# Performance work log

Hardware: AMD Instinct MI355X
Metric: run time of the kernel (lower is better)

## Reference

```python
import jax, jax.numpy as jnp
import numpy as np

BN_EPS = 1e-5

def _bn_train(h, gamma, beta):
    # BatchNorm1d in training mode: batch statistics over the node dim
    mean = jnp.mean(h, axis=0)
    var = jnp.mean((h - mean) ** 2, axis=0)  # biased variance, as torch BN uses for normalization
    return gamma * (h - mean) * jax.lax.rsqrt(var + BN_EPS) + beta


def setup_inputs() -> dict:
    key = jax.random.key(0)
    ks = jax.random.split(key, 8)
    N, E = 100000, 1250000
    d_in, d_out = 64, 128
    x = jax.random.normal(ks[0], (N, d_in), dtype=jnp.float32)
    edge_index = jax.random.randint(ks[1], (2, E), 0, N, dtype=jnp.int64)
    s1 = 1.0 / np.sqrt(d_in)
    s2 = 1.0 / np.sqrt(d_out)
    W1 = jax.random.uniform(ks[2], (d_in, d_out), dtype=jnp.float32, minval=-s1, maxval=s1)
    b1 = jax.random.uniform(ks[3], (d_out,), dtype=jnp.float32, minval=-s1, maxval=s1)
    g1 = jnp.ones((d_out,), dtype=jnp.float32)
    be1 = jnp.zeros((d_out,), dtype=jnp.float32)
    W2 = jax.random.uniform(ks[4], (d_out, d_out), dtype=jnp.float32, minval=-s2, maxval=s2)
    b2 = jax.random.uniform(ks[5], (d_out,), dtype=jnp.float32, minval=-s2, maxval=s2)
    g2 = jnp.ones((d_out,), dtype=jnp.float32)
    be2 = jnp.zeros((d_out,), dtype=jnp.float32)
    return {"x": x, "edge_index": edge_index, "W1": W1, "b1": b1, "g1": g1, "be1": be1,
            "W2": W2, "b2": b2, "g2": g2, "be2": be2}


def reference(x, edge_index, W1, b1, g1, be1, W2, b2, g2, be2):
    src = edge_index[0]
    dst = edge_index[1]
    N = x.shape[0]
    # GIN aggregation: sum of neighbor features scattered to destination nodes
    agg = jax.ops.segment_sum(x[src], dst, num_segments=N)
    h = x + agg  # (1 + eps) * x + agg with eps = 0 (GINConv default)
    # MLP: Linear -> ReLU -> BN -> Linear -> ReLU -> BN
    h = jnp.maximum(h @ W1 + b1, 0.0)
    h = _bn_train(h, g1, be1)
    h = jnp.maximum(h @ W2 + b2, 0.0)
    h = _bn_train(h, g2, be2)
    return h
```

## Files before the change

### kernel.cpp

```cpp
#include <hip/hip_runtime.h>


#define NBMAX 512
#define CAP   8192
#define CPB   4096

__global__ __launch_bounds__(512) void k_zero(int* __restrict__ gcnt,
                                              float* __restrict__ stats)
{
    int t = threadIdx.x;
    gcnt[t] = 0;
    stats[t] = 0.f;
}

__global__ __launch_bounds__(256) void k_part(const int* __restrict__ ei, int E,
                                              int* __restrict__ gcnt,
                                              unsigned int* __restrict__ pk)
{
    __shared__ int cnt[NBMAX];
    __shared__ int gbase[NBMAX];
    const int tid = threadIdx.x;
    const int e0 = blockIdx.x * CPB;
    const int e1 = min(E, e0 + CPB);

    for (int i = tid; i < NBMAX; i += 256) cnt[i] = 0;
    __syncthreads();

    for (int e = e0 + tid; e < e1; e += 256)
        atomicAdd(&cnt[ei[E + e] >> 8], 1);
    __syncthreads();

    for (int i = tid; i < NBMAX; i += 256)
        gbase[i] = cnt[i] ? atomicAdd(&gcnt[i], cnt[i]) : 0;
    __syncthreads();
    for (int i = tid; i < NBMAX; i += 256) cnt[i] = 0;
    __syncthreads();

    for (int e = e0 + tid; e < e1; e += 256) {
        int dst = ei[E + e];
        int src = ei[e];
        int b = dst >> 8;
        int lr = atomicAdd(&cnt[b], 1);
        pk[(long)b * CAP + gbase[b] + lr] =
            ((unsigned)(dst & 255) << 17) | (unsigned)src;
    }
}

__global__ __launch_bounds__(256) void k_csr(const unsigned int* __restrict__ pk,
                                             const int* __restrict__ gcnt,
                                             int* __restrict__ nbr,
                                             int* __restrict__ beg,
                                             int* __restrict__ endq, int N)
{
    __shared__ int lcnt[256];
    __shared__ int lscan[256];
    const int tid = threadIdx.x;
    const int b = blockIdx.x;
    const int cnt = gcnt[b];
    const unsigned int* eb = pk + (long)b * CAP;

    lcnt[tid] = 0;
    __syncthreads();
    for (int j = tid; j < cnt; j += 256)
        atomicAdd(&lcnt[eb[j] >> 17], 1);
    __syncthreads();

    int v = lcnt[tid];
    lscan[tid] = v;
    __syncthreads();
    for (int off = 1; off < 256; off <<= 1) {
        int t = (tid >= off) ? lscan[tid - off] : 0;
        __syncthreads();
        lscan[tid] += t;
        __syncthreads();
    }
    int excl = lscan[tid] - v;

    int node = (b << 8) + tid;
    if (node < N) {
        beg[node]  = b * CAP + excl;
        endq[node] = b * CAP + excl + v;
    }
    lcnt[tid] = excl;
    __syncthreads();

    for (int j = tid; j < cnt; j += 256) {
        unsigned int p = eb[j];
        int lr = atomicAdd(&lcnt[p >> 17], 1);
        nbr[b * CAP + lr] = (int)(p & 0x1FFFFu);
    }
}

__global__ __launch_bounds__(256) void k_gather(const float4* __restrict__ x4,
                                                const int* __restrict__ beg,
                                                const int* __restrict__ endq,
                                                const int* __restrict__ nbr,
                                                float4* __restrict__ h04, int N)
{
    int wid  = threadIdx.x >> 6;
    int lane = threadIdx.x & 63;
    int node = blockIdx.x * 4 + wid;
    if (node >= N) return;
    int d4 = lane & 15;
    int g  = lane >> 4;
    int b = beg[node], e = endq[node];

    float4 acc = make_float4(0.f, 0.f, 0.f, 0.f);
    if (g == 0) acc = x4[(long)node * 16 + d4];

    for (int j = b + g; j < e; j += 4) {
        int s = nbr[j];
        float4 v = x4[(long)s * 16 + d4];
        acc.x += v.x; acc.y += v.y; acc.z += v.z; acc.w += v.w;
    }

#pragma unroll
    for (int m = 16; m <= 32; m <<= 1) {
        acc.x += __shfl_xor(acc.x, m, 64);
        acc.y += __shfl_xor(acc.y, m, 64);
        acc.z += __shfl_xor(acc.z, m, 64);
        acc.w += __shfl_xor(acc.w, m, 64);
    }

    if (g == 0) h04[(long)node * 16 + d4] = acc;
}

template<int K>
__global__ __launch_bounds__(256) void k_gemm_bias_relu(
    const float* __restrict__ A, const float* __restrict__ W,
    const float* __restrict__ bias, float* __restrict__ Out, int N)
{
    __shared__ float sAT[64][72];
    __shared__ float sW[64][128];

    const int tid = threadIdx.x;
    const int tx = tid & 15;
    const int ty = tid >> 4;
    const int row0 = blockIdx.x * 64;

    float acc[4][8];
#pragma unroll
    for (int i = 0; i < 4; ++i)
#pragma unroll
        for (int j = 0; j < 8; ++j) acc[i][j] = 0.f;

    for (int k0 = 0; k0 < K; k0 += 64) {
#pragma unroll
        for (int ch = 0; ch < 4; ++ch) {
            int idx = ch * 256 + tid;
            int r = idx >> 4, kq = idx & 15;
            int grow = row0 + r;
            float4 v = make_float4(0.f, 0.f, 0.f, 0.f);
            if (grow < N) v = *(const float4*)(A + (long)grow * K + (k0 + kq * 4));
            sAT[kq * 4 + 0][r] = v.x;
            sAT[kq * 4 + 1][r] = v.y;
            sAT[kq * 4 + 2][r] = v.z;
            sAT[kq * 4 + 3][r] = v.w;
        }
#pragma unroll
        for (int ch = 0; ch < 8; ++ch) {
            int idx = ch * 256 + tid;
            int kr = idx >> 5, cq = idx & 31;
            *(float4*)(&sW[kr][cq * 4]) = *(const float4*)(W + (long)(k0 + kr) * 128 + cq * 4);
        }
        __syncthreads();

#pragma unroll 8
        for (int k = 0; k < 64; ++k) {
            float4 av = *(const float4*)(&sAT[k][ty * 4]);
            float4 w0 = *(const float4*)(&sW[k][tx * 4]);
            float4 w1 = *(const float4*)(&sW[k][64 + tx * 4]);
            float a[4] = {av.x, av.y, av.z, av.w};
            float w[8] = {w0.x, w0.y, w0.z, w0.w, w1.x, w1.y, w1.z, w1.w};
#pragma unroll
            for (int i = 0; i < 4; ++i)
#pragma unroll
                for (int j = 0; j < 8; ++j)
                    acc[i][j] = fmaf(a[i], w[j], acc[i][j]);
        }
        __syncthreads();
    }

    float b[8];
#pragma unroll
    for (int j = 0; j < 4; ++j) b[j] = bias[tx * 4 + j];
#pragma unroll
    for (int j = 0; j < 4; ++j) b[4 + j] = bias[64 + tx * 4 + j];

#pragma unroll
    for (int i = 0; i < 4; ++i) {
        int grow = row0 + ty * 4 + i;
        if (grow < N) {
            float4 o0, o1;
            o0.x = fmaxf(acc[i][0] + b[0], 0.f);
            o0.y = fmaxf(acc[i][1] + b[1], 0.f);
            o0.z = fmaxf(acc[i][2] + b[2], 0.f);
            o0.w = fmaxf(acc[i][3] + b[3], 0.f);
            o1.x = fmaxf(acc[i][4] + b[4], 0.f);
            o1.y = fmaxf(acc[i][5] + b[5], 0.f);
            o1.z = fmaxf(acc[i][6] + b[6], 0.f);
            o1.w = fmaxf(acc[i][7] + b[7], 0.f);
            *(float4*)(Out + (long)grow * 128 + tx * 4)      = o0;
            *(float4*)(Out + (long)grow * 128 + 64 + tx * 4) = o1;
        }
    }
}

__global__ __launch_bounds__(256) void k_col_stats(const float* __restrict__ H, int N,
                                                   float* __restrict__ sums,
                                                   float* __restrict__ sqs)
{
    int c = threadIdx.x & 127;
    int half = threadIdx.x >> 7;
    float s = 0.f, q = 0.f;
    for (long r = (long)blockIdx.x * 2 + half; r < N; r += (long)gridDim.x * 2) {
        float v = H[r * 128 + c];
        s += v;
        q = fmaf(v, v, q);
    }
    __shared__ float ls[256], lq[256];
    ls[threadIdx.x] = s;
    lq[threadIdx.x] = q;
    __syncthreads();
    if (threadIdx.x < 128) {
        atomicAdd(&sums[c], ls[threadIdx.x] + ls[threadIdx.x + 128]);
        atomicAdd(&sqs[c],  lq[threadIdx.x] + lq[threadIdx.x + 128]);
    }
}

__global__ void k_bn_fold(const float* __restrict__ stats,
                          const float* __restrict__ gamma, const float* __restrict__ beta,
                          const float* __restrict__ W2, const float* __restrict__ b2,
                          float* __restrict__ W2p, float* __restrict__ b2p, float invN)
{
    __shared__ float as[128], cs[128];
    int j = threadIdx.x;
    float m = stats[j] * invN;
    float v = stats[128 + j] * invN - m * m;
    float a = gamma[j] * rsqrtf(v + 1e-5f);
    float c = beta[j] - m * a;
    as[j] = a;
    cs[j] = c;
    __syncthreads();
    float bb = b2[j];
    for (int k = 0; k < 128; ++k) {
        float w = W2[k * 128 + j];
        W2p[k * 128 + j] = as[k] * w;
        bb = fmaf(cs[k], w, bb);
    }
    b2p[j] = bb;
}

__global__ void k_bn_coeffs(const float* __restrict__ stats,
                            const float* __restrict__ gamma, const float* __restrict__ beta,
                            float* __restrict__ ac, float invN)
{
    int j = threadIdx.x;
    float m = stats[j] * invN;
    float v = stats[128 + j] * invN - m * m;
    float a = gamma[j] * rsqrtf(v + 1e-5f);
    ac[j] = a;
    ac[128 + j] = beta[j] - m * a;
}

__global__ __launch_bounds__(256) void k_bn_apply(float* __restrict__ out,
                                                  const float* __restrict__ ac, long n4)
{
    __shared__ float sa[128], sc[128];
    if (threadIdx.x < 128) {
        sa[threadIdx.x] = ac[threadIdx.x];
        sc[threadIdx.x] = ac[128 + threadIdx.x];
    }
    __syncthreads();
    long i = (long)blockIdx.x * 256 + threadIdx.x;
    if (i < n4) {
        float4 v = ((float4*)out)[i];
        int c0 = (int)((i * 4) & 127);
        v.x = fmaf(v.x, sa[c0 + 0], sc[c0 + 0]);
        v.y = fmaf(v.y, sa[c0 + 1], sc[c0 + 1]);
        v.z = fmaf(v.z, sa[c0 + 2], sc[c0 + 2]);
        v.w = fmaf(v.w, sa[c0 + 3], sc[c0 + 3]);
        ((float4*)out)[i] = v;
    }
}

extern "C" void kernel_launch(void* const* d_in, const int* in_sizes, int n_in,
                              void* d_out, int out_size, void* d_ws, size_t ws_size,
                              hipStream_t stream)
{
    const float* x   = (const float*)d_in[0];
    const int*   ei  = (const int*)  d_in[1];
    const float* W1  = (const float*)d_in[2];
    const float* b1  = (const float*)d_in[3];
    const float* g1  = (const float*)d_in[4];
    const float* be1 = (const float*)d_in[5];
    const float* W2  = (const float*)d_in[6];
    const float* b2  = (const float*)d_in[7];
    const float* g2  = (const float*)d_in[8];
    const float* be2 = (const float*)d_in[9];
    float* out = (float*)d_out;

    const int N = in_sizes[0] / 64;
    const int E = in_sizes[1] / 2;
    const int nbuckets = (N + 255) >> 8;

    float* ws    = (float*)d_ws;
    float* h0    = ws;
    float* h1    = h0 + (long)N * 64;
    float* W2p   = h1 + (long)N * 128;
    float* b2p   = W2p + 128 * 128;
    float* stats = b2p + 128;
    float* ac    = stats + 512;
    int*   gcnt  = (int*)(ac + 256);

    unsigned int* pk  = (unsigned int*)h1;
    int*          nbr = (int*)h1 + (long)NBMAX * CAP;
    int*          beg = nbr + (long)NBMAX * CAP;
    int*          endq = beg + N;

    const float invN = 1.0f / (float)N;

    k_zero<<<1, 512, 0, stream>>>(gcnt, stats);

    k_part<<<(E + CPB - 1) / CPB, 256, 0, stream>>>(ei, E, gcnt, pk);

    k_csr<<<nbuckets, 256, 0, stream>>>(pk, gcnt, nbr, beg, endq, N);

    k_gather<<<(N + 3) / 4, 256, 0, stream>>>((const float4*)x, beg, endq, nbr,
                                              (float4*)h0, N);

    int gBlocks = (N + 63) / 64;
    k_gemm_bias_relu<64><<<gBlocks, 256, 0, stream>>>(h0, W1, b1, h1, N);

    k_col_stats<<<512, 256, 0, stream>>>(h1, N, stats, stats + 128);

    k_bn_fold<<<1, 128, 0, stream>>>(stats, g1, be1, W2, b2, W2p, b2p, invN);

    k_gemm_bias_relu<128><<<gBlocks, 256, 0, stream>>>(h1, W2p, b2p, out, N);

    k_col_stats<<<512, 256, 0, stream>>>(out, N, stats + 256, stats + 384);

    k_bn_coeffs<<<1, 128, 0, stream>>>(stats + 256, g2, be2, ac, invN);

    long n4o = (long)N * 128 / 4;
    k_bn_apply<<<(int)((n4o + 255) / 256), 256, 0, stream>>>(out, ac, n4o);
}
```

Measured before the change: 362.4 us.

## Fuse BatchNorm column statistics into GEMM epilogue and drop transposed A tile

The column sum and sum-of-squares reductions are computed in the GEMM epilogue: per-thread partials are reduced with wave shuffles, then shared-memory atomics, then one global atomic per column per block. This removes two separate k_col_stats passes that reread the N x 128 activations. The A tile is also stored row-major with float4 stores instead of a scalar transposed scatter, and the inner loop reads four A rows per 4-k step. In exchange there are far more global atomics (about 1563 blocks x 256 per GEMM), and LDS reads of A may now hit bank conflicts.

```diff
diff --git a/kernel.cpp b/kernel.cpp
--- a/kernel.cpp
+++ b/kernel.cpp
@@ -128,15 +128,19 @@
 template<int K>
 __global__ __launch_bounds__(256) void k_gemm_bias_relu(
     const float* __restrict__ A, const float* __restrict__ W,
-    const float* __restrict__ bias, float* __restrict__ Out, int N)
-{
-    __shared__ float sAT[64][72];
+    const float* __restrict__ bias, float* __restrict__ Out, int N,
+    float* __restrict__ sums, float* __restrict__ sqs)
+{
+    __shared__ float sA[64][68];
     __shared__ float sW[64][128];
+    __shared__ float lsum[128], lsq[128];
 
     const int tid = threadIdx.x;
     const int tx = tid & 15;
     const int ty = tid >> 4;
     const int row0 = blockIdx.x * 64;
+
+    if (tid < 128) { lsum[tid] = 0.f; lsq[tid] = 0.f; }
 
     float acc[4][8];
 #pragma unroll
@@ -152,10 +156,7 @@
             int grow = row0 + r;
             float4 v = make_float4(0.f, 0.f, 0.f, 0.f);
             if (grow < N) v = *(const float4*)(A + (long)grow * K + (k0 + kq * 4));
-            sAT[kq * 4 + 0][r] = v.x;
-            sAT[kq * 4 + 1][r] = v.y;
-            sAT[kq * 4 + 2][r] = v.z;
-            sAT[kq * 4 + 3][r] = v.w;
+            *(float4*)(&sA[r][kq * 4]) = v;
         }
 #pragma unroll
         for (int ch = 0; ch < 8; ++ch) {
@@ -165,18 +166,28 @@
         }
         __syncthreads();
 
-#pragma unroll 8
-        for (int k = 0; k < 64; ++k) {
-            float4 av = *(const float4*)(&sAT[k][ty * 4]);
-            float4 w0 = *(const float4*)(&sW[k][tx * 4]);
-            float4 w1 = *(const float4*)(&sW[k][64 + tx * 4]);
-            float a[4] = {av.x, av.y, av.z, av.w};
-            float w[8] = {w0.x, w0.y, w0.z, w0.w, w1.x, w1.y, w1.z, w1.w};
-#pragma unroll
-            for (int i = 0; i < 4; ++i)
-#pragma unroll
-                for (int j = 0; j < 8; ++j)
-                    acc[i][j] = fmaf(a[i], w[j], acc[i][j]);
+#pragma unroll 4
+        for (int k4 = 0; k4 < 16; ++k4) {
+            float4 a0 = *(const float4*)(&sA[ty * 4 + 0][k4 * 4]);
+            float4 a1 = *(const float4*)(&sA[ty * 4 + 1][k4 * 4]);
+            float4 a2 = *(const float4*)(&sA[ty * 4 + 2][k4 * 4]);
+            float4 a3 = *(const float4*)(&sA[ty * 4 + 3][k4 * 4]);
+            float ar[4][4] = {{a0.x, a0.y, a0.z, a0.w},
+                              {a1.x, a1.y, a1.z, a1.w},
+                              {a2.x, a2.y, a2.z, a2.w},
+                              {a3.x, a3.y, a3.z, a3.w}};
+#pragma unroll
+            for (int kk = 0; kk < 4; ++kk) {
+                int k = k4 * 4 + kk;
+                float4 w0 = *(const float4*)(&sW[k][tx * 4]);
+                float4 w1 = *(const float4*)(&sW[k][64 + tx * 4]);
+                float w[8] = {w0.x, w0.y, w0.z, w0.w, w1.x, w1.y, w1.z, w1.w};
+#pragma unroll
+                for (int i = 0; i < 4; ++i)
+#pragma unroll
+                    for (int j = 0; j < 8; ++j)
+                        acc[i][j] = fmaf(ar[i][kk], w[j], acc[i][j]);
+            }
         }
         __syncthreads();
     }
@@ -186,45 +197,49 @@
     for (int j = 0; j < 4; ++j) b[j] = bias[tx * 4 + j];
 #pragma unroll
     for (int j = 0; j < 4; ++j) b[4 + j] = bias[64 + tx * 4 + j];
+
+    float s[8], q[8];
+#pragma unroll
+    for (int j = 0; j < 8; ++j) { s[j] = 0.f; q[j] = 0.f; }
 
 #pragma unroll
     for (int i = 0; i < 4; ++i) {
         int grow = row0 + ty * 4 + i;
         if (grow < N) {
-            float4 o0, o1;
-            o0.x = fmaxf(acc[i][0] + b[0], 0.f);
-            o0.y = fmaxf(acc[i][1] + b[1], 0.f);
-            o0.z = fmaxf(acc[i][2] + b[2], 0.f);
-            o0.w = fmaxf(acc[i][3] + b[3], 0.f);
-            o1.x = fmaxf(acc[i][4] + b[4], 0.f);
-            o1.y = fmaxf(acc[i][5] + b[5], 0.f);
-            o1.z = fmaxf(acc[i][6] + b[6], 0.f);
-            o1.w = fmaxf(acc[i][7] + b[7], 0.f);
+            float o[8];
+#pragma unroll
+            for (int j = 0; j < 8; ++j) {
+                o[j] = fmaxf(acc[i][j] + b[j], 0.f);
+                s[j] += o[j];
+                q[j] = fmaf(o[j], o[j], q[j]);
+            }
+            float4 o0 = make_float4(o[0], o[1], o[2], o[3]);
+            float4 o1 = make_float4(o[4], o[5], o[6], o[7]);
             *(float4*)(Out + (long)grow * 128 + tx * 4)      = o0;
             *(float4*)(Out + (long)grow * 128 + 64 + tx * 4) = o1;
         }
     }
-}
-
-__global__ __launch_bounds__(256) void k_col_stats(const float* __restrict__ H, int N,
-                                                   float* __restrict__ sums,
-                                                   float* __restrict__ sqs)
-{
-    int c = threadIdx.x & 127;
-    int half = threadIdx.x >> 7;
-    float s = 0.f, q = 0.f;
-    for (long r = (long)blockIdx.x * 2 + half; r < N; r += (long)gridDim.x * 2) {
-        float v = H[r * 128 + c];
-        s += v;
-        q = fmaf(v, v, q);
-    }
-    __shared__ float ls[256], lq[256];
-    ls[threadIdx.x] = s;
-    lq[threadIdx.x] = q;
-    __syncthreads();
-    if (threadIdx.x < 128) {
-        atomicAdd(&sums[c], ls[threadIdx.x] + ls[threadIdx.x + 128]);
-        atomicAdd(&sqs[c],  lq[threadIdx.x] + lq[threadIdx.x + 128]);
+
+#pragma unroll
+    for (int j = 0; j < 8; ++j) {
+        s[j] += __shfl_xor(s[j], 16, 64);
+        s[j] += __shfl_xor(s[j], 32, 64);
+        q[j] += __shfl_xor(q[j], 16, 64);
+        q[j] += __shfl_xor(q[j], 32, 64);
+    }
+    if ((tid & 63) < 16) {
+#pragma unroll
+        for (int j = 0; j < 4; ++j) {
+            atomicAdd(&lsum[tx * 4 + j],      s[j]);
+            atomicAdd(&lsq [tx * 4 + j],      q[j]);
+            atomicAdd(&lsum[64 + tx * 4 + j], s[4 + j]);
+            atomicAdd(&lsq [64 + tx * 4 + j], q[4 + j]);
+        }
+    }
+    __syncthreads();
+    if (tid < 128) {
+        atomicAdd(&sums[tid], lsum[tid]);
+        atomicAdd(&sqs[tid],  lsq[tid]);
     }
 }
 
@@ -330,15 +345,13 @@
                                               (float4*)h0, N);
 
     int gBlocks = (N + 63) / 64;
-    k_gemm_bias_relu<64><<<gBlocks, 256, 0, stream>>>(h0, W1, b1, h1, N);
-
-    k_col_stats<<<512, 256, 0, stream>>>(h1, N, stats, stats + 128);
+    k_gemm_bias_relu<64><<<gBlocks, 256, 0, stream>>>(h0, W1, b1, h1, N,
+                                                      stats, stats + 128);
 
     k_bn_fold<<<1, 128, 0, stream>>>(stats, g1, be1, W2, b2, W2p, b2p, invN);
 
-    k_gemm_bias_relu<128><<<gBlocks, 256, 0, stream>>>(h1, W2p, b2p, out, N);
-
-    k_col_stats<<<512, 256, 0, stream>>>(out, N, stats + 256, stats + 384);
+    k_gemm_bias_relu<128><<<gBlocks, 256, 0, stream>>>(h1, W2p, b2p, out, N,
+                                                       stats + 256, stats + 384);
 
     k_bn_coeffs<<<1, 128, 0, stream>>>(stats + 256, g2, be2, ac, invN);
 
```

Result: faster. 330.3 us (-8.9%).
